# Optimization experiments

Measured on AMD Instinct MI355X. Metric: run time of the kernel, lower is better.

## Reference

```python
import jax, jax.numpy as jnp
import numpy as np

EPS = 1e-5

def _bn(x, gamma, beta):
    # training-mode BatchNorm1d over the batch axis (axis=1 of (K,B,H)), biased variance
    m = jnp.mean(x, axis=1, keepdims=True)
    v = jnp.mean((x - m) ** 2, axis=1, keepdims=True)
    return (x - m) * jax.lax.rsqrt(v + EPS) * gamma[:, None, :] + beta[:, None, :]

def setup_inputs() -> dict:
    key = jax.random.key(0)
    ks = jax.random.split(key, 20)
    B, T, D, H, K = 4096, 64, 256, 128, 12
    data_x = jax.random.randint(ks[0], (B, T, 1), 0, 2, dtype=jnp.int32)
    feats = jax.random.normal(ks[1], (B, T + 1, D), dtype=jnp.float32)
    s = 0.05
    return {
        "data_x": data_x,
        "feats": feats,
        "w_atom": jax.random.normal(ks[2], (K, D), jnp.float32) * s,
        "b_atom": jnp.zeros((K,), jnp.float32),
        "W1": jax.random.normal(ks[3], (K, D, H), jnp.float32) * s,
        "b1": jnp.zeros((K, H), jnp.float32),
        "g1": jnp.ones((K, H), jnp.float32),
        "be1": jnp.zeros((K, H), jnp.float32),
        "W2": jax.random.normal(ks[4], (K, H, H), jnp.float32) * s,
        "b2": jnp.zeros((K, H), jnp.float32),
        "g2": jnp.ones((K, H), jnp.float32),
        "be2": jnp.zeros((K, H), jnp.float32),
        "W3": jax.random.normal(ks[5], (K, H, H), jnp.float32) * s,
        "b3": jnp.zeros((K, H), jnp.float32),
        "g3": jnp.ones((K, H), jnp.float32),
        "be3": jnp.zeros((K, H), jnp.float32),
        "Wout": jax.random.normal(ks[6], (K, H), jnp.float32) * s,
        "bout": jnp.zeros((K,), jnp.float32),
    }

def reference(data_x, feats, w_atom, b_atom, W1, b1, g1, be1, W2, b2, g2, be2, W3, b3, g3, be3, Wout, bout):
    # valid-node mask: padding where data_x[:,:,0]==0
    valid = (data_x[:, :, 0] != 0).astype(feats.dtype)          # (B,T)
    f = feats[:, 1:, :]                                          # (B,T,D)
    # per-task atom importance weights (sigmoid(Linear(D,1)))
    w = jax.nn.sigmoid(jnp.einsum('btd,kd->kbt', f, w_atom) + b_atom[:, None, None])  # (K,B,T)
    # weighted segment-sum readout per molecule (sum_nodes with weight 'w' over valid atoms)
    mol = jnp.einsum('kbt,bt,btd->kbd', w, valid, f)             # (K,B,D)
    # per-task MLP heads: Dropout(0)->Linear->ReLU->BatchNorm1d, x3, then Linear(H,1)
    h1 = _bn(jax.nn.relu(jnp.einsum('kbd,kdh->kbh', mol, W1) + b1[:, None, :]), g1, be1)
    h2 = _bn(jax.nn.relu(jnp.einsum('kbh,khj->kbj', h1, W2) + b2[:, None, :]), g2, be2)
    h3 = _bn(jax.nn.relu(jnp.einsum('kbh,khj->kbj', h2, W3) + b3[:, None, :]), g3, be3)
    pred = jnp.einsum('kbh,kh->kb', h3, Wout) + bout[:, None]    # (K,B)
    prediction_all = pred.T                                      # (B,K) = torch.cat over tasks
    atom_weights = w * valid[None, :, :]                         # (K,B,T), dense-padded atom weight list
    return (prediction_all, atom_weights)
```

## Files before the change

### kernel.cpp

```cpp
#include <hip/hip_runtime.h>
#include <hip/hip_bf16.h>

#define B_N 4096
#define T_N 64
#define D_N 256
#define H_N 128
#define K_N 12

typedef __attribute__((ext_vector_type(8))) short short8;
typedef __attribute__((ext_vector_type(4))) float f32x4;

static __device__ __forceinline__ unsigned bf16_rne(float x) {
  unsigned u = __float_as_uint(x);
  return (u + 0x7fffu + ((u >> 16) & 1u)) >> 16;
}
static __device__ __forceinline__ unsigned pk2(float a, float b) {
  return bf16_rne(a) | (bf16_rne(b) << 16);
}
static __device__ __forceinline__ float lo16(unsigned u) { return __uint_as_float(u << 16); }
static __device__ __forceinline__ float hi16(unsigned u) { return __uint_as_float(u & 0xffff0000u); }

__global__ void prep_wa(const float* __restrict__ w_atom, unsigned* __restrict__ wa_frag) {
  const int tid = blockIdx.x * 64 + threadIdx.x;
  const int s = tid >> 6, l = tid & 63;
  const int k = l & 15, h = l >> 4, d0 = s * 32 + h * 8;
  unsigned o[4];
#pragma unroll
  for (int j = 0; j < 4; ++j) {
    const float a = (k < K_N) ? w_atom[k * D_N + d0 + 2 * j]     : 0.f;
    const float b = (k < K_N) ? w_atom[k * D_N + d0 + 2 * j + 1] : 0.f;
    o[j] = pk2(a, b);
  }
  *(uint4*)(wa_frag + (size_t)tid * 4) = make_uint4(o[0], o[1], o[2], o[3]);
}

__global__ void prep_w(const float* __restrict__ W, unsigned* __restrict__ out, int S) {
  const int id = blockIdx.x * 256 + threadIdx.x;
  const int total = K_N * 8 * S * 64;
  if (id >= total) return;
  const int lane = id & 63;
  const int s  = (id >> 6) % S;
  const int nt = ((id >> 6) / S) & 7;
  const int kk = id / (64 * S * 8);
  const int n  = nt * 16 + (lane & 15);
  const int d0 = 32 * s + 8 * (lane >> 4);
  const int D  = 32 * S;
  unsigned o[4];
#pragma unroll
  for (int j = 0; j < 4; ++j) {
    const float a = W[(size_t)kk * D * H_N + (d0 + 2 * j) * H_N + n];
    const float b = W[(size_t)kk * D * H_N + (d0 + 2 * j + 1) * H_N + n];
    o[j] = pk2(a, b);
  }
  *(uint4*)(out + (size_t)id * 4) = make_uint4(o[0], o[1], o[2], o[3]);
}

__global__ __launch_bounds__(256, 4) void k1_mol(
    const int* __restrict__ dx, const float* __restrict__ feats,
    const unsigned* __restrict__ wa_frag, const float* __restrict__ b_atom,
    float* __restrict__ out_atom, unsigned* __restrict__ molb)
{
  __shared__ unsigned tile[64 * 128];
  __shared__ float dxv[64];
  __shared__ float wv32[K_N * 64];

  const int tid  = threadIdx.x;
  const int lane = tid & 63;
  const int w    = tid >> 6;
  const int b    = blockIdx.x;
  const int k    = lane & 15;
  const int h    = lane >> 4;

  short8 bfr[8];
  {
    const short8* wf8 = (const short8*)wa_frag;
#pragma unroll
    for (int s = 0; s < 8; ++s) bfr[s] = wf8[s * 64 + lane];
  }
  const float ba = (k < K_N) ? b_atom[k] : 0.f;
  if (tid < 64) dxv[tid] = (dx[b * T_N + tid] != 0) ? 1.f : 0.f;

  {
    const float* fg0 = feats + ((size_t)b * 65 + 1) * 256
                     + (size_t)(16 * w) * 256 + 4 * lane;
    float4 rr[8];
#pragma unroll
    for (int i = 0; i < 8; ++i) rr[i] = *(const float4*)(fg0 + (size_t)i * 256);
#pragma unroll
    for (int i = 0; i < 16; ++i) {
      const float4 v = rr[i & 7];
      if (i < 8) rr[i & 7] = *(const float4*)(fg0 + (size_t)(i + 8) * 256);
      const int t = 16 * w + i;
      const unsigned off = t * 128 + (((lane >> 1) ^ i) << 2) + (lane & 1) * 2;
      *(uint2*)&tile[off] = make_uint2(pk2(v.x, v.y), pk2(v.z, v.w));
    }
  }
  __syncthreads();

  f32x4 cacc = {0.f, 0.f, 0.f, 0.f};
#pragma unroll
  for (int s = 0; s < 8; ++s) {
    const unsigned off = (16 * w + k) * 128 + (((4 * s + h) ^ k) << 2);
    const short8 afrag = *(const short8*)&tile[off];
    cacc = __builtin_amdgcn_mfma_f32_16x16x32_bf16(afrag, bfr[s], cacc, 0, 0, 0);
  }

#pragma unroll
  for (int r = 0; r < 4; ++r) {
    const int tl = 4 * h + r;
    const float valid = dxv[16 * w + tl];
    const float wv = valid / (1.f + __expf(-(cacc[r] + ba)));
    if (k < K_N) wv32[k * 64 + 16 * w + tl] = wv;
  }
  __syncthreads();

  const int kb = w * 3;
  float4 m0 = make_float4(0.f, 0.f, 0.f, 0.f), m1 = m0, m2 = m0;
#pragma unroll
  for (int tc = 0; tc < 16; ++tc) {
    const float4 wv0 = *(const float4*)&wv32[(kb + 0) * 64 + (tc << 2)];
    const float4 wv1 = *(const float4*)&wv32[(kb + 1) * 64 + (tc << 2)];
    const float4 wv2 = *(const float4*)&wv32[(kb + 2) * 64 + (tc << 2)];
    const float w0a[4] = {wv0.x, wv0.y, wv0.z, wv0.w};
    const float w1a[4] = {wv1.x, wv1.y, wv1.z, wv1.w};
    const float w2a[4] = {wv2.x, wv2.y, wv2.z, wv2.w};
#pragma unroll
    for (int j = 0; j < 4; ++j) {
      const int t = (tc << 2) + j;
      const unsigned off = t * 128 + (((lane >> 1) ^ (t & 15)) << 2) + (lane & 1) * 2;
      const uint2 pw = *(const uint2*)&tile[off];
      const float f0 = lo16(pw.x), f1 = hi16(pw.x);
      const float f2 = lo16(pw.y), f3 = hi16(pw.y);
      m0.x = fmaf(w0a[j], f0, m0.x); m0.y = fmaf(w0a[j], f1, m0.y);
      m0.z = fmaf(w0a[j], f2, m0.z); m0.w = fmaf(w0a[j], f3, m0.w);
      m1.x = fmaf(w1a[j], f0, m1.x); m1.y = fmaf(w1a[j], f1, m1.y);
      m1.z = fmaf(w1a[j], f2, m1.z); m1.w = fmaf(w1a[j], f3, m1.w);
      m2.x = fmaf(w2a[j], f0, m2.x); m2.y = fmaf(w2a[j], f1, m2.y);
      m2.z = fmaf(w2a[j], f2, m2.z); m2.w = fmaf(w2a[j], f3, m2.w);
    }
  }
  unsigned* mpb = molb + ((size_t)kb * B_N + b) * 128 + (lane << 1);
  *(uint2*)(mpb)                      = make_uint2(pk2(m0.x, m0.y), pk2(m0.z, m0.w));
  *(uint2*)(mpb + (size_t)B_N * 128)  = make_uint2(pk2(m1.x, m1.y), pk2(m1.z, m1.w));
  *(uint2*)(mpb + (size_t)2 * B_N * 128) = make_uint2(pk2(m2.x, m2.y), pk2(m2.z, m2.w));

  if (tid < 192) {
    const float4 v = *(const float4*)&wv32[tid * 4];
    const int kk = tid >> 4, t0 = (tid & 15) * 4;
    *(float4*)&out_atom[((size_t)kk * B_N + b) * T_N + t0] = v;
  }
}

template <int S, bool AFFINE>
__global__ __launch_bounds__(256) void gemm_mfma(
    const unsigned* __restrict__ Abf, const unsigned* __restrict__ wpack,
    const float* __restrict__ bias, const float* __restrict__ alpha,
    const float* __restrict__ beta, unsigned short* __restrict__ Hout,
    float* __restrict__ ssum, float* __restrict__ ssq)
{
  __shared__ unsigned tile[64 * S * 16];
  __shared__ float redS[4][8][16];
  __shared__ float redQ[4][8][16];

  const int k   = blockIdx.y;
  const int b0  = blockIdx.x << 6;
  const int tid = threadIdx.x;
  const int lane = tid & 63;
  const int wv  = tid >> 6;
  const int ln15 = lane & 15;
  const int hq   = lane >> 4;

  {
    const int row = tid >> 2, q = tid & 3;
    const uint4* Ar = (const uint4*)Abf + ((size_t)k * B_N + b0 + row) * (S * 4) + q * S;
#pragma unroll
    for (int gi = 0; gi < S; ++gi) {
      const int g = q * S + gi;
      uint4 u = Ar[gi];
      if (AFFINE) {
        const float4 al0 = *(const float4*)(alpha + k * H_N + g * 8);
        const float4 al1 = *(const float4*)(alpha + k * H_N + g * 8 + 4);
        const float4 bt0 = *(const float4*)(beta  + k * H_N + g * 8);
        const float4 bt1 = *(const float4*)(beta  + k * H_N + g * 8 + 4);
        u.x = pk2(fmaf(lo16(u.x), al0.x, bt0.x), fmaf(hi16(u.x), al0.y, bt0.y));
        u.y = pk2(fmaf(lo16(u.y), al0.z, bt0.z), fmaf(hi16(u.y), al0.w, bt0.w));
        u.z = pk2(fmaf(lo16(u.z), al1.x, bt1.x), fmaf(hi16(u.z), al1.y, bt1.y));
        u.w = pk2(fmaf(lo16(u.w), al1.z, bt1.z), fmaf(hi16(u.w), al1.w, bt1.w));
      }
      *(uint4*)&tile[row * (S * 16) + ((g ^ (row & 15)) << 2)] = u;
    }
  }
  __syncthreads();

  const short8* wp8 = (const short8*)wpack + (size_t)k * 8 * S * 64 + lane;
  f32x4 acc[8];
#pragma unroll
  for (int nt = 0; nt < 8; ++nt) acc[nt] = (f32x4){0.f, 0.f, 0.f, 0.f};

  short8 bs0[8], bs1[8];
#pragma unroll
  for (int nt = 0; nt < 8; ++nt) bs0[nt] = wp8[(nt * S) * 64];
#pragma unroll
  for (int s = 0; s < S; ++s) {
    if (s + 1 < S) {
#pragma unroll
      for (int nt = 0; nt < 8; ++nt) {
        if (s & 1) bs0[nt] = wp8[(nt * S + s + 1) * 64];
        else       bs1[nt] = wp8[(nt * S + s + 1) * 64];
      }
    }
    const int arow = (wv << 4) + ln15;
    const unsigned aoff = arow * (S * 16) + (((4 * s + hq) ^ ln15) << 2);
    const short8 af = *(const short8*)&tile[aoff];
#pragma unroll
    for (int nt = 0; nt < 8; ++nt) {
      const short8 bf = (s & 1) ? bs1[nt] : bs0[nt];
      acc[nt] = __builtin_amdgcn_mfma_f32_16x16x32_bf16(af, bf, acc[nt], 0, 0, 0);
    }
  }

#pragma unroll
  for (int nt = 0; nt < 8; ++nt) {
    const int col = nt * 16 + ln15;
    const float bv = bias[k * H_N + col];
    float cs = 0.f, cq = 0.f;
#pragma unroll
    for (int r = 0; r < 4; ++r) {
      const float o = fmaxf(acc[nt][r] + bv, 0.f);
      cs += o; cq = fmaf(o, o, cq);
      const int row = b0 + (wv << 4) + (hq << 2) + r;
      Hout[((size_t)k * B_N + row) * H_N + col] = (unsigned short)bf16_rne(o);
    }
    cs += __shfl_xor(cs, 16); cs += __shfl_xor(cs, 32);
    cq += __shfl_xor(cq, 16); cq += __shfl_xor(cq, 32);
    if (lane < 16) { redS[wv][nt][ln15] = cs; redQ[wv][nt][ln15] = cq; }
  }
  __syncthreads();
  if (tid < 128) {
    const int nt = tid >> 4, c = tid & 15;
    float s = 0.f, q = 0.f;
#pragma unroll
    for (int i = 0; i < 4; ++i) { s += redS[i][nt][c]; q += redQ[i][nt][c]; }
    atomicAdd(&ssum[k * H_N + nt * 16 + c], s);
    atomicAdd(&ssq[k * H_N + nt * 16 + c], q);
  }
}

__global__ void bn_coef(const float* __restrict__ ssum, const float* __restrict__ ssq,
                        const float* __restrict__ g, const float* __restrict__ be,
                        float* __restrict__ alpha, float* __restrict__ beta)
{
  const int i = blockIdx.x * 256 + threadIdx.x;
  if (i >= K_N * H_N) return;
  const float inv_n = 1.f / (float)B_N;
  const float m = ssum[i] * inv_n;
  float v = fmaf(ssq[i], inv_n, -m * m);
  v = fmaxf(v, 0.f);
  const float a = g[i] * rsqrtf(v + 1e-5f);
  alpha[i] = a;
  beta[i]  = fmaf(-m, a, be[i]);
}

__global__ __launch_bounds__(256) void k_pred(
    const unsigned* __restrict__ h3, const float* __restrict__ alpha,
    const float* __restrict__ beta, const float* __restrict__ Wout,
    const float* __restrict__ bout, float* __restrict__ out)
{
  const int lane = threadIdx.x & 63;
  const int wv   = threadIdx.x >> 6;
  const int pair = blockIdx.x * 4 + wv;
  const int b = pair / K_N, k = pair - b * K_N;
  const unsigned xp = h3[((size_t)k * B_N + b) * 64 + lane];
  const float2 al = *(const float2*)(alpha + k * H_N + (lane << 1));
  const float2 be = *(const float2*)(beta  + k * H_N + (lane << 1));
  const float2 wo = *(const float2*)(Wout  + k * H_N + (lane << 1));
  float s = fmaf(lo16(xp), al.x, be.x) * wo.x + fmaf(hi16(xp), al.y, be.y) * wo.y;
#pragma unroll
  for (int off = 32; off; off >>= 1) s += __shfl_down(s, off);
  if (lane == 0) out[pair] = s + bout[k];
}

extern "C" void kernel_launch(void* const* d_in, const int* in_sizes, int n_in,
                              void* d_out, int out_size, void* d_ws, size_t ws_size,
                              hipStream_t stream)
{
  (void)in_sizes; (void)n_in; (void)out_size; (void)ws_size;
  const int*   dx     = (const int*)d_in[0];
  const float* feats  = (const float*)d_in[1];
  const float* w_atom = (const float*)d_in[2];
  const float* b_atom = (const float*)d_in[3];
  const float* W1 = (const float*)d_in[4];
  const float* b1 = (const float*)d_in[5];
  const float* g1 = (const float*)d_in[6];
  const float* be1 = (const float*)d_in[7];
  const float* W2 = (const float*)d_in[8];
  const float* b2 = (const float*)d_in[9];
  const float* g2 = (const float*)d_in[10];
  const float* be2 = (const float*)d_in[11];
  const float* W3 = (const float*)d_in[12];
  const float* b3 = (const float*)d_in[13];
  const float* g3 = (const float*)d_in[14];
  const float* be3 = (const float*)d_in[15];
  const float* Wout = (const float*)d_in[16];
  const float* bout = (const float*)d_in[17];

  float* out      = (float*)d_out;
  float* pred_out = out;
  float* atom_out = out + (size_t)B_N * K_N;

  char* wsb = (char*)d_ws;
  unsigned*       molb = (unsigned*)wsb;
  unsigned short* h1   = (unsigned short*)(wsb + 25165824);
  unsigned short* h2   = (unsigned short*)(wsb + 37748736);
  unsigned short* h3   = (unsigned short*)(wsb + 50331648);
  float* st = (float*)(wsb + 62914560);
  float* s1 = st,        *q1 = st + 1536;
  float* s2 = st + 3072, *q2 = st + 4608;
  float* s3 = st + 6144, *q3 = st + 7680;
  float* ab = st + 9216;
  float* al1 = ab,        *bt1 = ab + 1536;
  float* al2 = ab + 3072, *bt2 = ab + 4608;
  float* al3 = ab + 6144, *bt3 = ab + 7680;
  unsigned* wa_frag = (unsigned*)(ab + 9216);
  unsigned* w1p = wa_frag + 2048;
  unsigned* w2p = w1p + 196608;
  unsigned* w3p = w2p + 98304;

  hipMemsetAsync(st, 0, 6 * 1536 * sizeof(float), stream);

  prep_wa<<<8, 64, 0, stream>>>(w_atom, wa_frag);
  prep_w<<<(K_N * 8 * 8 * 64 + 255) / 256, 256, 0, stream>>>(W1, w1p, 8);
  prep_w<<<(K_N * 8 * 4 * 64 + 255) / 256, 256, 0, stream>>>(W2, w2p, 4);
  prep_w<<<(K_N * 8 * 4 * 64 + 255) / 256, 256, 0, stream>>>(W3, w3p, 4);

  k1_mol<<<B_N, 256, 0, stream>>>(dx, feats, wa_frag, b_atom, atom_out, molb);

  gemm_mfma<8, false><<<dim3(64, 12), 256, 0, stream>>>(
      molb, w1p, b1, nullptr, nullptr, h1, s1, q1);
  bn_coef<<<6, 256, 0, stream>>>(s1, q1, g1, be1, al1, bt1);
  gemm_mfma<4, true><<<dim3(64, 12), 256, 0, stream>>>(
      (const unsigned*)h1, w2p, b2, al1, bt1, h2, s2, q2);
  bn_coef<<<6, 256, 0, stream>>>(s2, q2, g2, be2, al2, bt2);
  gemm_mfma<4, true><<<dim3(64, 12), 256, 0, stream>>>(
      (const unsigned*)h2, w3p, b3, al2, bt2, h3, s3, q3);
  bn_coef<<<6, 256, 0, stream>>>(s3, q3, g3, be3, al3, bt3);
  k_pred<<<B_N * K_N / 4, 256, 0, stream>>>(
      (const unsigned*)h3, al3, bt3, Wout, bout, pred_out);
}
```

Before: 150.5 us.

## Warp-specialize k1_mol into producer/consumer waves with double-buffered LDS tiles

k1_mol now uses 512-thread blocks that each process 8 molecules. Four producer waves load the next molecule's features into a double-buffered LDS tile while four consumer waves run the MFMA atom-weight and weighted-sum stages on the current tile. The goal is to overlap global feature loads with compute and to amortize the weight-fragment loads across molecules. The cost is LDS doubling to two tiles, more barrier traffic, and a grid of only 512 blocks, which may reduce occupancy and hurt latency hiding.

```diff
diff --git a/kernel.cpp b/kernel.cpp
--- a/kernel.cpp
+++ b/kernel.cpp
@@ -55,99 +55,126 @@
   *(uint4*)(out + (size_t)id * 4) = make_uint4(o[0], o[1], o[2], o[3]);
 }
 
-__global__ __launch_bounds__(256, 4) void k1_mol(
+__global__ __launch_bounds__(512, 4) void k1_mol(
     const int* __restrict__ dx, const float* __restrict__ feats,
     const unsigned* __restrict__ wa_frag, const float* __restrict__ b_atom,
     float* __restrict__ out_atom, unsigned* __restrict__ molb)
 {
-  __shared__ unsigned tile[64 * 128];
-  __shared__ float dxv[64];
+  __shared__ unsigned tile[2][64 * 128];
   __shared__ float wv32[K_N * 64];
 
   const int tid  = threadIdx.x;
   const int lane = tid & 63;
   const int w    = tid >> 6;
-  const int b    = blockIdx.x;
-  const int k    = lane & 15;
-  const int h    = lane >> 4;
-
-  short8 bfr[8];
-  {
-    const short8* wf8 = (const short8*)wa_frag;
-#pragma unroll
-    for (int s = 0; s < 8; ++s) bfr[s] = wf8[s * 64 + lane];
-  }
-  const float ba = (k < K_N) ? b_atom[k] : 0.f;
-  if (tid < 64) dxv[tid] = (dx[b * T_N + tid] != 0) ? 1.f : 0.f;
-
-  {
-    const float* fg0 = feats + ((size_t)b * 65 + 1) * 256
-                     + (size_t)(16 * w) * 256 + 4 * lane;
-    float4 rr[8];
-#pragma unroll
-    for (int i = 0; i < 8; ++i) rr[i] = *(const float4*)(fg0 + (size_t)i * 256);
-#pragma unroll
-    for (int i = 0; i < 16; ++i) {
-      const float4 v = rr[i & 7];
-      if (i < 8) rr[i & 7] = *(const float4*)(fg0 + (size_t)(i + 8) * 256);
-      const int t = 16 * w + i;
-      const unsigned off = t * 128 + (((lane >> 1) ^ i) << 2) + (lane & 1) * 2;
-      *(uint2*)&tile[off] = make_uint2(pk2(v.x, v.y), pk2(v.z, v.w));
-    }
-  }
-  __syncthreads();
-
-  f32x4 cacc = {0.f, 0.f, 0.f, 0.f};
-#pragma unroll
-  for (int s = 0; s < 8; ++s) {
-    const unsigned off = (16 * w + k) * 128 + (((4 * s + h) ^ k) << 2);
-    const short8 afrag = *(const short8*)&tile[off];
-    cacc = __builtin_amdgcn_mfma_f32_16x16x32_bf16(afrag, bfr[s], cacc, 0, 0, 0);
-  }
-
-#pragma unroll
-  for (int r = 0; r < 4; ++r) {
-    const int tl = 4 * h + r;
-    const float valid = dxv[16 * w + tl];
-    const float wv = valid / (1.f + __expf(-(cacc[r] + ba)));
-    if (k < K_N) wv32[k * 64 + 16 * w + tl] = wv;
-  }
-  __syncthreads();
-
-  const int kb = w * 3;
-  float4 m0 = make_float4(0.f, 0.f, 0.f, 0.f), m1 = m0, m2 = m0;
-#pragma unroll
-  for (int tc = 0; tc < 16; ++tc) {
-    const float4 wv0 = *(const float4*)&wv32[(kb + 0) * 64 + (tc << 2)];
-    const float4 wv1 = *(const float4*)&wv32[(kb + 1) * 64 + (tc << 2)];
-    const float4 wv2 = *(const float4*)&wv32[(kb + 2) * 64 + (tc << 2)];
-    const float w0a[4] = {wv0.x, wv0.y, wv0.z, wv0.w};
-    const float w1a[4] = {wv1.x, wv1.y, wv1.z, wv1.w};
-    const float w2a[4] = {wv2.x, wv2.y, wv2.z, wv2.w};
-#pragma unroll
-    for (int j = 0; j < 4; ++j) {
-      const int t = (tc << 2) + j;
-      const unsigned off = t * 128 + (((lane >> 1) ^ (t & 15)) << 2) + (lane & 1) * 2;
-      const uint2 pw = *(const uint2*)&tile[off];
-      const float f0 = lo16(pw.x), f1 = hi16(pw.x);
-      const float f2 = lo16(pw.y), f3 = hi16(pw.y);
-      m0.x = fmaf(w0a[j], f0, m0.x); m0.y = fmaf(w0a[j], f1, m0.y);
-      m0.z = fmaf(w0a[j], f2, m0.z); m0.w = fmaf(w0a[j], f3, m0.w);
-      m1.x = fmaf(w1a[j], f0, m1.x); m1.y = fmaf(w1a[j], f1, m1.y);
-      m1.z = fmaf(w1a[j], f2, m1.z); m1.w = fmaf(w1a[j], f3, m1.w);
-      m2.x = fmaf(w2a[j], f0, m2.x); m2.y = fmaf(w2a[j], f1, m2.y);
-      m2.z = fmaf(w2a[j], f2, m2.z); m2.w = fmaf(w2a[j], f3, m2.w);
-    }
-  }
-  unsigned* mpb = molb + ((size_t)kb * B_N + b) * 128 + (lane << 1);
-  *(uint2*)(mpb)                      = make_uint2(pk2(m0.x, m0.y), pk2(m0.z, m0.w));
-  *(uint2*)(mpb + (size_t)B_N * 128)  = make_uint2(pk2(m1.x, m1.y), pk2(m1.z, m1.w));
-  *(uint2*)(mpb + (size_t)2 * B_N * 128) = make_uint2(pk2(m2.x, m2.y), pk2(m2.z, m2.w));
-
-  if (tid < 192) {
-    const float4 v = *(const float4*)&wv32[tid * 4];
-    const int kk = tid >> 4, t0 = (tid & 15) * 4;
-    *(float4*)&out_atom[((size_t)kk * B_N + b) * T_N + t0] = v;
+  const int b0   = blockIdx.x * 8;
+
+  if (w < 4) {
+    const int pw = w;
+    const size_t rowbase = (size_t)(16 * pw) * 256 + 4 * lane;
+    float4 r[16];
+
+    {
+      const float* fg = feats + ((size_t)b0 * 65 + 1) * 256 + rowbase;
+#pragma unroll
+      for (int i = 0; i < 16; ++i) r[i] = *(const float4*)(fg + (size_t)i * 256);
+#pragma unroll
+      for (int i = 0; i < 16; ++i) {
+        const unsigned off = (16 * pw + i) * 128 + (((lane >> 1) ^ i) << 2) + (lane & 1) * 2;
+        *(uint2*)&tile[0][off] = make_uint2(pk2(r[i].x, r[i].y), pk2(r[i].z, r[i].w));
+      }
+      asm volatile("s_waitcnt lgkmcnt(0)" ::: "memory");
+      __builtin_amdgcn_s_barrier();
+    }
+
+    for (int ib = 0; ib < 8; ++ib) {
+      if (ib + 1 < 8) {
+        const float* fg = feats + ((size_t)(b0 + ib + 1) * 65 + 1) * 256 + rowbase;
+#pragma unroll
+        for (int i = 0; i < 16; ++i) r[i] = *(const float4*)(fg + (size_t)i * 256);
+      }
+      __builtin_amdgcn_s_barrier();
+      if (ib + 1 < 8) {
+        unsigned* dst = &tile[(ib + 1) & 1][0];
+#pragma unroll
+        for (int i = 0; i < 16; ++i) {
+          const unsigned off = (16 * pw + i) * 128 + (((lane >> 1) ^ i) << 2) + (lane & 1) * 2;
+          *(uint2*)&dst[off] = make_uint2(pk2(r[i].x, r[i].y), pk2(r[i].z, r[i].w));
+        }
+      }
+      asm volatile("s_waitcnt lgkmcnt(0)" ::: "memory");
+      __builtin_amdgcn_s_barrier();
+    }
+  } else {
+    const int cw = w - 4;
+    const int k = lane & 15, h = lane >> 4;
+    short8 bfr[8];
+    {
+      const short8* wf8 = (const short8*)wa_frag;
+#pragma unroll
+      for (int s = 0; s < 8; ++s) bfr[s] = wf8[s * 64 + lane];
+    }
+    const float ba = (k < K_N) ? b_atom[k] : 0.f;
+    __builtin_amdgcn_s_barrier();
+
+    for (int ib = 0; ib < 8; ++ib) {
+      const int b = b0 + ib;
+      const unsigned* tl = &tile[ib & 1][0];
+      const int4 dvv = *(const int4*)(dx + b * T_N + 16 * cw + 4 * h);
+
+      f32x4 cacc = {0.f, 0.f, 0.f, 0.f};
+#pragma unroll
+      for (int s = 0; s < 8; ++s) {
+        const unsigned off = (16 * cw + k) * 128 + (((4 * s + h) ^ k) << 2);
+        const short8 af = *(const short8*)&tl[off];
+        cacc = __builtin_amdgcn_mfma_f32_16x16x32_bf16(af, bfr[s], cacc, 0, 0, 0);
+      }
+#pragma unroll
+      for (int rr = 0; rr < 4; ++rr) {
+        const float valid = (((const int*)&dvv)[rr] != 0) ? 1.f : 0.f;
+        const float wvv = valid / (1.f + __expf(-(cacc[rr] + ba)));
+        if (k < K_N) wv32[k * 64 + 16 * cw + 4 * h + rr] = wvv;
+      }
+      asm volatile("s_waitcnt lgkmcnt(0)" ::: "memory");
+      __builtin_amdgcn_s_barrier();
+
+      const int kb = cw * 3;
+      float4 m0 = make_float4(0.f, 0.f, 0.f, 0.f), m1 = m0, m2 = m0;
+#pragma unroll
+      for (int tc = 0; tc < 16; ++tc) {
+        const float4 wv0 = *(const float4*)&wv32[(kb + 0) * 64 + (tc << 2)];
+        const float4 wv1 = *(const float4*)&wv32[(kb + 1) * 64 + (tc << 2)];
+        const float4 wv2 = *(const float4*)&wv32[(kb + 2) * 64 + (tc << 2)];
+        const float w0a[4] = {wv0.x, wv0.y, wv0.z, wv0.w};
+        const float w1a[4] = {wv1.x, wv1.y, wv1.z, wv1.w};
+        const float w2a[4] = {wv2.x, wv2.y, wv2.z, wv2.w};
+#pragma unroll
+        for (int j = 0; j < 4; ++j) {
+          const int t = (tc << 2) + j;
+          const unsigned off = t * 128 + (((lane >> 1) ^ (t & 15)) << 2) + (lane & 1) * 2;
+          const uint2 pw2 = *(const uint2*)&tl[off];
+          const float f0 = lo16(pw2.x), f1 = hi16(pw2.x);
+          const float f2 = lo16(pw2.y), f3 = hi16(pw2.y);
+          m0.x = fmaf(w0a[j], f0, m0.x); m0.y = fmaf(w0a[j], f1, m0.y);
+          m0.z = fmaf(w0a[j], f2, m0.z); m0.w = fmaf(w0a[j], f3, m0.w);
+          m1.x = fmaf(w1a[j], f0, m1.x); m1.y = fmaf(w1a[j], f1, m1.y);
+          m1.z = fmaf(w1a[j], f2, m1.z); m1.w = fmaf(w1a[j], f3, m1.w);
+          m2.x = fmaf(w2a[j], f0, m2.x); m2.y = fmaf(w2a[j], f1, m2.y);
+          m2.z = fmaf(w2a[j], f2, m2.z); m2.w = fmaf(w2a[j], f3, m2.w);
+        }
+      }
+      unsigned* mpb = molb + ((size_t)kb * B_N + b) * 128 + (lane << 1);
+      *(uint2*)(mpb)                         = make_uint2(pk2(m0.x, m0.y), pk2(m0.z, m0.w));
+      *(uint2*)(mpb + (size_t)B_N * 128)     = make_uint2(pk2(m1.x, m1.y), pk2(m1.z, m1.w));
+      *(uint2*)(mpb + (size_t)2 * B_N * 128) = make_uint2(pk2(m2.x, m2.y), pk2(m2.z, m2.w));
+
+      const int ctid = tid - 256;
+      if (ctid < 192) {
+        const float4 v = *(const float4*)&wv32[ctid * 4];
+        const int kk = ctid >> 4, t0 = (ctid & 15) * 4;
+        *(float4*)&out_atom[((size_t)kk * B_N + b) * T_N + t0] = v;
+      }
+      __builtin_amdgcn_s_barrier();
+    }
   }
 }
 
@@ -333,7 +360,7 @@
   prep_w<<<(K_N * 8 * 4 * 64 + 255) / 256, 256, 0, stream>>>(W2, w2p, 4);
   prep_w<<<(K_N * 8 * 4 * 64 + 255) / 256, 256, 0, stream>>>(W3, w3p, 4);
 
-  k1_mol<<<B_N, 256, 0, stream>>>(dx, feats, wa_frag, b_atom, atom_out, molb);
+  k1_mol<<<B_N / 8, 512, 0, stream>>>(dx, feats, wa_frag, b_atom, atom_out, molb);
 
   gemm_mfma<8, false><<<dim3(64, 12), 256, 0, stream>>>(
       molb, w1p, b1, nullptr, nullptr, h1, s1, q1);
```

Result: slower. 186.9 us (+24.2%).
